# Performance work log

Hardware: AMD Instinct MI355X
Metric: run time of the kernel (lower is better)

The kernel has to match this reference:

```python
import jax, jax.numpy as jnp
import numpy as np

B = 4096        # batch
T = 365         # encoder sequence length
H = 64          # hidden size
HORIZON = 7


def setup_inputs() -> dict:
    key = jax.random.key(0)
    ks = jax.random.split(key, 16)
    s = 0.05
    w = lambda k, shape: (jax.random.normal(k, shape, dtype=jnp.float32) * s)
    return {
        "x": jax.random.normal(ks[0], (B, T, 1), dtype=jnp.float32),
        "enc_Wih0": w(ks[1], (4 * H, 1)),
        "enc_Whh0": w(ks[2], (4 * H, H)),
        "enc_b0": w(ks[3], (4 * H,)),
        "enc_Wih1": w(ks[4], (4 * H, H)),
        "enc_Whh1": w(ks[5], (4 * H, H)),
        "enc_b1": w(ks[6], (4 * H,)),
        "dec_Wih0": w(ks[7], (4 * H, 1)),
        "dec_Whh0": w(ks[8], (4 * H, H)),
        "dec_b0": w(ks[9], (4 * H,)),
        "dec_Wih1": w(ks[10], (4 * H, H)),
        "dec_Whh1": w(ks[11], (4 * H, H)),
        "dec_b1": w(ks[12], (4 * H,)),
        "fc_W": w(ks[13], (1, H)),
        "fc_b": w(ks[14], (1,)),
    }


def _lstm_cell(xt, h, c, Wih, Whh, b):
    # PyTorch gate order: input, forget, cell(g), output
    gates = xt @ Wih.T + h @ Whh.T + b  # [B, 4H]
    i, f, g, o = jnp.split(gates, 4, axis=-1)
    c_new = jax.nn.sigmoid(f) * c + jax.nn.sigmoid(i) * jnp.tanh(g)
    h_new = jax.nn.sigmoid(o) * jnp.tanh(c_new)
    return h_new, c_new


def _run_layer(seq, Wih, Whh, b):
    # seq: [T, B, in] -> hidden seq [T, B, H], final (h, c)
    bsz = seq.shape[1]
    h0 = jnp.zeros((bsz, H), seq.dtype)
    c0 = jnp.zeros((bsz, H), seq.dtype)

    def step(carry, xt):
        h, c = carry
        h, c = _lstm_cell(xt, h, c, Wih, Whh, b)
        return (h, c), h

    (hF, cF), hs = jax.lax.scan(step, (h0, c0), seq)
    return hs, hF, cF


def reference(x, enc_Wih0, enc_Whh0, enc_b0, enc_Wih1, enc_Whh1, enc_b1,
              dec_Wih0, dec_Whh0, dec_b0, dec_Wih1, dec_Whh1, dec_b1,
              fc_W, fc_b):
    xT = jnp.transpose(x, (1, 0, 2))  # [T, B, 1]
    hs0, h0, c0 = _run_layer(xT, enc_Wih0, enc_Whh0, enc_b0)
    _, h1, c1 = _run_layer(hs0, enc_Wih1, enc_Whh1, enc_b1)

    dec_in = jnp.zeros((x.shape[0], 1), x.dtype)  # [B, 1]
    outs = []
    for _ in range(HORIZON):
        h0, c0 = _lstm_cell(dec_in, h0, c0, dec_Wih0, dec_Whh0, dec_b0)
        h1, c1 = _lstm_cell(h0, h1, c1, dec_Wih1, dec_Whh1, dec_b1)
        pred = h1 @ fc_W.T + fc_b  # [B, 1]
        outs.append(pred)
        dec_in = pred
    return jnp.stack(outs, axis=1)  # [B, HORIZON, 1]
```

## Files before the change

kernel.cpp:

```cpp
#include <hip/hip_runtime.h>


typedef _Float16 f16x8 __attribute__((ext_vector_type(8)));
typedef _Float16 f16x4 __attribute__((ext_vector_type(4)));
typedef float    f32x4 __attribute__((ext_vector_type(4)));
typedef float    f32x2 __attribute__((ext_vector_type(2)));

static constexpr int T_ENC = 365;
static constexpr int HZ    = 7;
static constexpr int BT    = 16;
static constexpr int HPAD  = 72;

static constexpr float LOG2E  = 1.442695040888963f;
static constexpr float SCL_I  = -LOG2E;
static constexpr float SCL_G  = 2.0f * LOG2E;

#if __has_builtin(__builtin_amdgcn_exp2f)
__device__ __forceinline__ float fexp2(float x) { return __builtin_amdgcn_exp2f(x); }
#else
__device__ __forceinline__ float fexp2(float x) { return __exp2f(x); }
#endif
#if __has_builtin(__builtin_amdgcn_rcpf)
__device__ __forceinline__ float frcp(float x) { return __builtin_amdgcn_rcpf(x); }
#else
__device__ __forceinline__ float frcp(float x) { return 1.0f / x; }
#endif

__device__ __forceinline__ f32x4 mm1(f16x8 w, f16x8 a, f32x4 acc) {
  return __builtin_amdgcn_mfma_f32_16x16x32_f16(w, a, acc, 0, 0, 0);
}

__global__ __launch_bounds__(512, 2)
void lstm_fused(const float* __restrict__ x,
                const float* __restrict__ eWih0, const float* __restrict__ eWhh0,
                const float* __restrict__ eb0,
                const float* __restrict__ eWih1, const float* __restrict__ eWhh1,
                const float* __restrict__ eb1,
                const float* __restrict__ dWih0, const float* __restrict__ dWhh0,
                const float* __restrict__ db0,
                const float* __restrict__ dWih1, const float* __restrict__ dWhh1,
                const float* __restrict__ db1,
                const float* __restrict__ fcW, const float* __restrict__ fcb,
                float* __restrict__ out)
{
  __shared__ __align__(16) float    xs[T_ENC * BT];
  __shared__ __align__(16) _Float16 h0s[2][BT * HPAD];
  __shared__ __align__(16) _Float16 h1s[2][BT * HPAD];
  __shared__ __align__(16) float    pp[2][16 * 256];
  __shared__ __align__(16) float    dins[BT];

  const int tid  = threadIdx.x;
  const int lane = tid & 63;
  const int wv   = tid >> 6;
  const int wg   = wv & 3;
  const int n    = lane & 15;
  const int q    = lane >> 4;
  const int b0g  = blockIdx.x * BT;
  const int nH   = n * HPAD;
  const int cbase = (wg << 4) + (q << 2);
  const int ppswz = (n & 7) << 2;
  const int ppn   = n << 8;

#if __has_builtin(__builtin_amdgcn_s_setprio)
  if (wv >= 4) __builtin_amdgcn_s_setprio(1);
#endif

  for (int i = tid; i < T_ENC * BT; i += 512) {
    int b = i / T_ENC;
    int t = i - b * T_ENC;
    xs[t * BT + b] = x[(b0g + b) * T_ENC + t];
  }
  for (int i = tid; i < 2 * BT * HPAD; i += 512) {
    ((_Float16*)h0s)[i] = (_Float16)0.f;
    ((_Float16*)h1s)[i] = (_Float16)0.f;
  }
  if (tid < BT) dins[tid] = 0.f;

  f16x8 WA[4][2], WB[4][2], WP[4][2];
  f32x4 biasq[4], wih0q[4], biasqP[4];

  auto gscale = [&](int ti) { return (ti == 2) ? SCL_G : SCL_I; };

  auto cvtrow = [&](const float* p, float s, f16x8& w) {
    #pragma unroll
    for (int j = 0; j < 8; ++j) w[j] = (_Float16)(p[j] * s);
  };
  auto loadA = [&](const float* Wih0_, const float* Whh0_, const float* b0_) {
    #pragma unroll
    for (int ti = 0; ti < 4; ++ti) {
      const float s = gscale(ti);
      const int rw = (ti * 4 + wg) * 16 + n;
      const int rq = (ti * 4 + wg) * 16 + (q << 2);
      #pragma unroll
      for (int rr = 0; rr < 4; ++rr) {
        biasq[ti][rr] = b0_[rq + rr] * s;
        wih0q[ti][rr] = Wih0_[rq + rr] * s;
      }
      #pragma unroll
      for (int kc = 0; kc < 2; ++kc)
        cvtrow(Whh0_ + rw * 64 + kc * 32 + q * 8, s, WA[ti][kc]);
    }
  };
  auto loadAP = [&](const float* Wih1_, const float* b1_) {
    #pragma unroll
    for (int ti = 0; ti < 4; ++ti) {
      const float s = gscale(ti);
      const int rw = (ti * 4 + wg) * 16 + n;
      const int rq = (ti * 4 + wg) * 16 + (q << 2);
      #pragma unroll
      for (int rr = 0; rr < 4; ++rr) biasqP[ti][rr] = b1_[rq + rr] * s;
      #pragma unroll
      for (int kc = 0; kc < 2; ++kc)
        cvtrow(Wih1_ + rw * 64 + kc * 32 + q * 8, s, WP[ti][kc]);
    }
  };
  auto loadB = [&](const float* Wih1_, const float* Whh1_, const float* b1_) {
    #pragma unroll
    for (int ti = 0; ti < 4; ++ti) {
      const float s = gscale(ti);
      const int rw = (ti * 4 + wg) * 16 + n;
      const int rq = (ti * 4 + wg) * 16 + (q << 2);
      #pragma unroll
      for (int rr = 0; rr < 4; ++rr) biasq[ti][rr] = b1_[rq + rr] * s;
      #pragma unroll
      for (int kc = 0; kc < 2; ++kc) {
        cvtrow(Wih1_ + rw * 64 + kc * 32 + q * 8, s, WA[ti][kc]);
        cvtrow(Whh1_ + rw * 64 + kc * 32 + q * 8, s, WB[ti][kc]);
      }
    }
  };

  if (wv < 4) { loadA(eWih0, eWhh0, eb0); loadAP(eWih1, eb1); }
  else        loadB(eWih1, eWhh1, eb1);

  f32x2 cp[2] = {{0.f, 0.f}, {0.f, 0.f}};

  auto act2 = [&](f32x2 a0, f32x2 a1, f32x2 a2, f32x2 a3, f32x2& c) -> f32x2 {
    f32x2 ei, ef, eg, eo;
    ei.x = fexp2(a0.x); ei.y = fexp2(a0.y);
    ef.x = fexp2(a1.x); ef.y = fexp2(a1.y);
    eg.x = fexp2(a2.x); eg.y = fexp2(a2.y);
    eo.x = fexp2(a3.x); eo.y = fexp2(a3.y);
    const f32x2 one = {1.f, 1.f};
    f32x2 di = one + ei, df = one + ef, dg = one + eg, dd = one + eo;
    f32x2 dif = di * df;
    f32x2 dic = di * c;
    f32x2 t1  = dif * dg;
    f32x2 nd  = eg * df - df;
    f32x2 pc  = dic * dg;
    f32x2 s   = pc + nd;
    const f32x2 sclg = {SCL_G, SCL_G};
    f32x2 sg  = sclg * s;
    f32x2 R1; R1.x = frcp(t1.x); R1.y = frcp(t1.y);
    c = R1 * s;
    f32x2 ca = R1 * sg;
    const f32x2 cap = {20.f, 20.f};
    ca.x = fminf(ca.x, cap.x); ca.y = fminf(ca.y, cap.y);
    f32x2 ec; ec.x = fexp2(ca.x); ec.y = fexp2(ca.y);
    f32x2 t2 = ec * dd + dd;
    f32x2 nc = ec - one;
    f32x2 R2; R2.x = frcp(t2.x); R2.y = frcp(t2.y);
    return nc * R2;
  };

  auto epilogue = [&](const f32x4* g, _Float16* O) {
    f32x2 h2[2];
    #pragma unroll
    for (int pr = 0; pr < 2; ++pr) {
      f32x2 a0 = {g[0][2 * pr], g[0][2 * pr + 1]};
      f32x2 a1 = {g[1][2 * pr], g[1][2 * pr + 1]};
      f32x2 a2 = {g[2][2 * pr], g[2][2 * pr + 1]};
      f32x2 a3 = {g[3][2 * pr], g[3][2 * pr + 1]};
      h2[pr] = act2(a0, a1, a2, a3, cp[pr]);
    }
    f16x4 hv;
    hv[0] = (_Float16)h2[0].x; hv[1] = (_Float16)h2[0].y;
    hv[2] = (_Float16)h2[1].x; hv[3] = (_Float16)h2[1].y;
    *(f16x4*)(O + nH + cbase) = hv;
  };

  auto stepA = [&](const _Float16* H, _Float16* O, float xb) {
    const _Float16* hp = H + nH;
    f16x8 a0 = *(const f16x8*)(hp + q * 8);
    f16x8 a1 = *(const f16x8*)(hp + 32 + q * 8);
    const f32x4 xbv = {xb, xb, xb, xb};
    f32x4 g[4];
    #pragma unroll
    for (int ti = 0; ti < 4; ++ti) {
      f32x4 ci = biasq[ti] + xbv * wih0q[ti];
      f32x4 a = mm1(WA[ti][0], a0, ci);
      a = mm1(WA[ti][1], a1, a);
      g[ti] = a;
    }
    epilogue(g, O);
  };

  auto stepAP = [&](const _Float16* H, _Float16* O, float xb, float* ppb) {
    const _Float16* hp = H + nH;
    f16x8 a0 = *(const f16x8*)(hp + q * 8);
    f16x8 a1 = *(const f16x8*)(hp + 32 + q * 8);
    const f32x4 xbv = {xb, xb, xb, xb};
    f32x4 g[4];
    #pragma unroll
    for (int ti = 0; ti < 4; ++ti) {
      f32x4 ci = biasq[ti] + xbv * wih0q[ti];
      f32x4 a = mm1(WA[ti][0], a0, ci);
      a = mm1(WA[ti][1], a1, a);
      g[ti] = a;
    }
    #pragma unroll
    for (int ti = 0; ti < 4; ++ti) {
      f32x4 p = mm1(WP[ti][0], a0, biasqP[ti]);
      p = mm1(WP[ti][1], a1, p);
      const int rq = ((ti * 4 + wg) << 4) + (q << 2);
      *(f32x4*)&ppb[ppn + (rq ^ ppswz)] = p;
    }
    epilogue(g, O);
  };

  auto partialOnly = [&](const _Float16* H, float* ppb) {
    const _Float16* hp = H + nH;
    f16x8 a0 = *(const f16x8*)(hp + q * 8);
    f16x8 a1 = *(const f16x8*)(hp + 32 + q * 8);
    #pragma unroll
    for (int ti = 0; ti < 4; ++ti) {
      f32x4 p = mm1(WP[ti][0], a0, biasqP[ti]);
      p = mm1(WP[ti][1], a1, p);
      const int rq = ((ti * 4 + wg) << 4) + (q << 2);
      *(f32x4*)&ppb[ppn + (rq ^ ppswz)] = p;
    }
  };

  auto stepB_enc = [&](const _Float16* H1, const float* ppb, _Float16* O) {
    const _Float16* p1 = H1 + nH;
    f16x8 a0 = *(const f16x8*)(p1 + q * 8);
    f16x8 a1 = *(const f16x8*)(p1 + 32 + q * 8);
    f32x4 g[4];
    #pragma unroll
    for (int ti = 0; ti < 4; ++ti) {
      const int rq = ((ti * 4 + wg) << 4) + (q << 2);
      f32x4 ci = *(const f32x4*)&ppb[ppn + (rq ^ ppswz)];
      f32x4 a = mm1(WB[ti][0], a0, ci);
      a = mm1(WB[ti][1], a1, a);
      g[ti] = a;
    }
    epilogue(g, O);
  };

  auto stepB = [&](const _Float16* H0, const _Float16* H1, _Float16* O) {
    const _Float16* p0 = H0 + nH;
    const _Float16* p1 = H1 + nH;
    f16x8 b0 = *(const f16x8*)(p0 + q * 8);
    f16x8 b1 = *(const f16x8*)(p0 + 32 + q * 8);
    f16x8 a0 = *(const f16x8*)(p1 + q * 8);
    f16x8 a1 = *(const f16x8*)(p1 + 32 + q * 8);
    f32x4 g[4];
    #pragma unroll
    for (int ti = 0; ti < 4; ++ti) {
      f32x4 a = mm1(WA[ti][0], b0, biasq[ti]);
      a = mm1(WA[ti][1], b1, a);
      a = mm1(WB[ti][0], a0, a);
      a = mm1(WB[ti][1], a1, a);
      g[ti] = a;
    }
    epilogue(g, O);
  };

  __syncthreads();

  float* pp0 = pp[0];
  float* pp1 = pp[1];

  float xb_next;
  if (wv < 4) {
    stepA(h0s[1], h0s[0], xs[n]);
    xb_next = xs[BT + n];
  }
  __syncthreads();
  if (wv < 4) {
    stepAP(h0s[0], h0s[1], xb_next, pp0);
    xb_next = xs[2 * BT + n];
  }
  __syncthreads();

  for (int s = 2; s <= 362; s += 2) {
    if (wv < 4) {
      stepAP(h0s[1], h0s[0], xb_next, pp1);
      xb_next = xs[(s + 1) * BT + n];
    } else {
      stepB_enc(h1s[1], pp0, h1s[0]);
    }
    __syncthreads();
    if (wv < 4) {
      stepAP(h0s[0], h0s[1], xb_next, pp0);
      xb_next = xs[(s + 2) * BT + n];
    } else {
      stepB_enc(h1s[0], pp1, h1s[1]);
    }
    __syncthreads();
  }

  if (wv < 4) stepAP(h0s[1], h0s[0], xb_next, pp1);
  else        stepB_enc(h1s[1], pp0, h1s[0]);
  __syncthreads();
  if (wv < 4) partialOnly(h0s[0], pp0);
  else        stepB_enc(h1s[0], pp1, h1s[1]);
  __syncthreads();
  if (wv < 4) loadA(dWih0, dWhh0, db0);
  else        stepB_enc(h1s[1], pp0, h1s[0]);
  __syncthreads();

  if (wv >= 4) loadB(dWih1, dWhh1, db1);
  float fcw[16];
  #pragma unroll
  for (int j = 0; j < 16; ++j) fcw[j] = fcW[q * 16 + j];
  const float fcb0 = fcb[0];

  #pragma unroll 1
  for (int hz = 0; hz < HZ; ++hz) {
    const int p = hz & 1;
    if (wv < 4) {
      stepA(h0s[p], h0s[1 - p], dins[n]);
    }
    __syncthreads();
    if (wv >= 4) {
      stepB(h0s[1 - p], h1s[p], h1s[1 - p]);
    }
    __syncthreads();
    if (wv == 0) {
      const _Float16* Hh = h1s[1 - p];
      f16x8 hh0 = *(const f16x8*)(Hh + nH + q * 16);
      f16x8 hh1 = *(const f16x8*)(Hh + nH + q * 16 + 8);
      float pacc = 0.f;
      #pragma unroll
      for (int j = 0; j < 8; ++j) pacc += fcw[j] * (float)hh0[j];
      #pragma unroll
      for (int j = 0; j < 8; ++j) pacc += fcw[8 + j] * (float)hh1[j];
      pacc += __shfl_down(pacc, 32);
      pacc += __shfl_down(pacc, 16);
      if (lane < BT) {
        pacc += fcb0;
        out[(b0g + lane) * HZ + hz] = pacc;
        dins[lane] = pacc;
      }
    }
    __syncthreads();
  }
}

extern "C" void kernel_launch(void* const* d_in, const int* in_sizes, int n_in,
                              void* d_out, int out_size, void* d_ws, size_t ws_size,
                              hipStream_t stream) {
  (void)in_sizes; (void)n_in; (void)d_ws; (void)ws_size; (void)out_size;
  const float* x     = (const float*)d_in[0];
  const float* eWih0 = (const float*)d_in[1];
  const float* eWhh0 = (const float*)d_in[2];
  const float* eb0   = (const float*)d_in[3];
  const float* eWih1 = (const float*)d_in[4];
  const float* eWhh1 = (const float*)d_in[5];
  const float* eb1   = (const float*)d_in[6];
  const float* dWih0 = (const float*)d_in[7];
  const float* dWhh0 = (const float*)d_in[8];
  const float* db0   = (const float*)d_in[9];
  const float* dWih1 = (const float*)d_in[10];
  const float* dWhh1 = (const float*)d_in[11];
  const float* db1   = (const float*)d_in[12];
  const float* fcW   = (const float*)d_in[13];
  const float* fcb   = (const float*)d_in[14];
  float* out = (float*)d_out;

  dim3 grid(4096 / BT);
  dim3 block(512);
  hipLaunchKernelGGL(lstm_fused, grid, block, 0, stream,
                     x, eWih0, eWhh0, eb0, eWih1, eWhh1, eb1,
                     dWih0, dWhh0, db0, dWih1, dWhh1, db1, fcW, fcb, out);
}
```

Measured before the change: 323.5 us.

## Split layer-1 input projection into a third wave group of 768-thread blocks

Block size grows from 512 to 768 threads. A new group of four waves computes the layer-1 input projection (Wih1·h0 plus bias) into the shared partial buffer, so the layer-0 waves only run their own recurrence step and register use per wave drops (WP/biasqP removed, weights share a WX slot). This shortens the per-step critical path of the layer-0 waves. The costs are more waves contending for the MFMA units and barriers, launch bounds of 768×3 that may limit registers or occupancy, and a setprio change that now raises priority for waves 0–7.

```diff
diff --git a/kernel.cpp b/kernel.cpp
--- a/kernel.cpp
+++ b/kernel.cpp
@@ -30,7 +30,7 @@
   return __builtin_amdgcn_mfma_f32_16x16x32_f16(w, a, acc, 0, 0, 0);
 }
 
-__global__ __launch_bounds__(512, 2)
+__global__ __launch_bounds__(768, 3)
 void lstm_fused(const float* __restrict__ x,
                 const float* __restrict__ eWih0, const float* __restrict__ eWhh0,
                 const float* __restrict__ eb0,
@@ -62,22 +62,22 @@
   const int ppn   = n << 8;
 
 #if __has_builtin(__builtin_amdgcn_s_setprio)
-  if (wv >= 4) __builtin_amdgcn_s_setprio(1);
+  if (wv < 8) __builtin_amdgcn_s_setprio(1);
 #endif
 
-  for (int i = tid; i < T_ENC * BT; i += 512) {
+  for (int i = tid; i < T_ENC * BT; i += 768) {
     int b = i / T_ENC;
     int t = i - b * T_ENC;
     xs[t * BT + b] = x[(b0g + b) * T_ENC + t];
   }
-  for (int i = tid; i < 2 * BT * HPAD; i += 512) {
+  for (int i = tid; i < 2 * BT * HPAD; i += 768) {
     ((_Float16*)h0s)[i] = (_Float16)0.f;
     ((_Float16*)h1s)[i] = (_Float16)0.f;
   }
   if (tid < BT) dins[tid] = 0.f;
 
-  f16x8 WA[4][2], WB[4][2], WP[4][2];
-  f32x4 biasq[4], wih0q[4], biasqP[4];
+  f16x8 WA[4][2], WX[4][2];
+  f32x4 biasq[4], wih0q[4];
 
   auto gscale = [&](int ti) { return (ti == 2) ? SCL_G : SCL_I; };
 
@@ -101,17 +101,27 @@
         cvtrow(Whh0_ + rw * 64 + kc * 32 + q * 8, s, WA[ti][kc]);
     }
   };
-  auto loadAP = [&](const float* Wih1_, const float* b1_) {
+  auto loadWhh = [&](const float* Whh1_) {
+    #pragma unroll
+    for (int ti = 0; ti < 4; ++ti) {
+      const float s = gscale(ti);
+      const int rw = (ti * 4 + wg) * 16 + n;
+      #pragma unroll
+      for (int kc = 0; kc < 2; ++kc)
+        cvtrow(Whh1_ + rw * 64 + kc * 32 + q * 8, s, WX[ti][kc]);
+    }
+  };
+  auto loadWP = [&](const float* Wih1_, const float* b1_) {
     #pragma unroll
     for (int ti = 0; ti < 4; ++ti) {
       const float s = gscale(ti);
       const int rw = (ti * 4 + wg) * 16 + n;
       const int rq = (ti * 4 + wg) * 16 + (q << 2);
       #pragma unroll
-      for (int rr = 0; rr < 4; ++rr) biasqP[ti][rr] = b1_[rq + rr] * s;
+      for (int rr = 0; rr < 4; ++rr) biasq[ti][rr] = b1_[rq + rr] * s;
       #pragma unroll
       for (int kc = 0; kc < 2; ++kc)
-        cvtrow(Wih1_ + rw * 64 + kc * 32 + q * 8, s, WP[ti][kc]);
+        cvtrow(Wih1_ + rw * 64 + kc * 32 + q * 8, s, WX[ti][kc]);
     }
   };
   auto loadB = [&](const float* Wih1_, const float* Whh1_, const float* b1_) {
@@ -125,13 +135,14 @@
       #pragma unroll
       for (int kc = 0; kc < 2; ++kc) {
         cvtrow(Wih1_ + rw * 64 + kc * 32 + q * 8, s, WA[ti][kc]);
-        cvtrow(Whh1_ + rw * 64 + kc * 32 + q * 8, s, WB[ti][kc]);
+        cvtrow(Whh1_ + rw * 64 + kc * 32 + q * 8, s, WX[ti][kc]);
       }
     }
   };
 
-  if (wv < 4) { loadA(eWih0, eWhh0, eb0); loadAP(eWih1, eb1); }
-  else        loadB(eWih1, eWhh1, eb1);
+  if (wv < 4)      loadA(eWih0, eWhh0, eb0);
+  else if (wv < 8) loadWhh(eWhh1);
+  else             loadWP(eWih1, eb1);
 
   f32x2 cp[2] = {{0.f, 0.f}, {0.f, 0.f}};
 
@@ -195,43 +206,20 @@
     epilogue(g, O);
   };
 
-  auto stepAP = [&](const _Float16* H, _Float16* O, float xb, float* ppb) {
+  auto stepP = [&](const _Float16* H, float* ppb) {
     const _Float16* hp = H + nH;
     f16x8 a0 = *(const f16x8*)(hp + q * 8);
     f16x8 a1 = *(const f16x8*)(hp + 32 + q * 8);
-    const f32x4 xbv = {xb, xb, xb, xb};
-    f32x4 g[4];
-    #pragma unroll
-    for (int ti = 0; ti < 4; ++ti) {
-      f32x4 ci = biasq[ti] + xbv * wih0q[ti];
-      f32x4 a = mm1(WA[ti][0], a0, ci);
-      a = mm1(WA[ti][1], a1, a);
-      g[ti] = a;
-    }
-    #pragma unroll
-    for (int ti = 0; ti < 4; ++ti) {
-      f32x4 p = mm1(WP[ti][0], a0, biasqP[ti]);
-      p = mm1(WP[ti][1], a1, p);
+    #pragma unroll
+    for (int ti = 0; ti < 4; ++ti) {
+      f32x4 p = mm1(WX[ti][0], a0, biasq[ti]);
+      p = mm1(WX[ti][1], a1, p);
       const int rq = ((ti * 4 + wg) << 4) + (q << 2);
       *(f32x4*)&ppb[ppn + (rq ^ ppswz)] = p;
     }
-    epilogue(g, O);
-  };
-
-  auto partialOnly = [&](const _Float16* H, float* ppb) {
-    const _Float16* hp = H + nH;
-    f16x8 a0 = *(const f16x8*)(hp + q * 8);
-    f16x8 a1 = *(const f16x8*)(hp + 32 + q * 8);
-    #pragma unroll
-    for (int ti = 0; ti < 4; ++ti) {
-      f32x4 p = mm1(WP[ti][0], a0, biasqP[ti]);
-      p = mm1(WP[ti][1], a1, p);
-      const int rq = ((ti * 4 + wg) << 4) + (q << 2);
-      *(f32x4*)&ppb[ppn + (rq ^ ppswz)] = p;
-    }
-  };
-
-  auto stepB_enc = [&](const _Float16* H1, const float* ppb, _Float16* O) {
+  };
+
+  auto stepB2 = [&](const _Float16* H1, const float* ppb, _Float16* O) {
     const _Float16* p1 = H1 + nH;
     f16x8 a0 = *(const f16x8*)(p1 + q * 8);
     f16x8 a1 = *(const f16x8*)(p1 + 32 + q * 8);
@@ -240,8 +228,8 @@
     for (int ti = 0; ti < 4; ++ti) {
       const int rq = ((ti * 4 + wg) << 4) + (q << 2);
       f32x4 ci = *(const f32x4*)&ppb[ppn + (rq ^ ppswz)];
-      f32x4 a = mm1(WB[ti][0], a0, ci);
-      a = mm1(WB[ti][1], a1, a);
+      f32x4 a = mm1(WX[ti][0], a0, ci);
+      a = mm1(WX[ti][1], a1, a);
       g[ti] = a;
     }
     epilogue(g, O);
@@ -259,8 +247,8 @@
     for (int ti = 0; ti < 4; ++ti) {
       f32x4 a = mm1(WA[ti][0], b0, biasq[ti]);
       a = mm1(WA[ti][1], b1, a);
-      a = mm1(WB[ti][0], a0, a);
-      a = mm1(WB[ti][1], a1, a);
+      a = mm1(WX[ti][0], a0, a);
+      a = mm1(WX[ti][1], a1, a);
       g[ti] = a;
     }
     epilogue(g, O);
@@ -278,39 +266,46 @@
   }
   __syncthreads();
   if (wv < 4) {
-    stepAP(h0s[0], h0s[1], xb_next, pp0);
+    stepA(h0s[0], h0s[1], xb_next);
     xb_next = xs[2 * BT + n];
-  }
-  __syncthreads();
-
-  for (int s = 2; s <= 362; s += 2) {
+  } else if (wv >= 8) {
+    stepP(h0s[0], pp0);
+  }
+  __syncthreads();
+
+  for (int u = 2; u <= 362; u += 2) {
     if (wv < 4) {
-      stepAP(h0s[1], h0s[0], xb_next, pp1);
-      xb_next = xs[(s + 1) * BT + n];
+      stepA(h0s[1], h0s[0], xb_next);
+      xb_next = xs[(u + 1) * BT + n];
+    } else if (wv < 8) {
+      stepB2(h1s[1], pp0, h1s[0]);
     } else {
-      stepB_enc(h1s[1], pp0, h1s[0]);
+      stepP(h0s[1], pp1);
     }
     __syncthreads();
     if (wv < 4) {
-      stepAP(h0s[0], h0s[1], xb_next, pp0);
-      xb_next = xs[(s + 2) * BT + n];
+      stepA(h0s[0], h0s[1], xb_next);
+      xb_next = xs[(u + 2) * BT + n];
+    } else if (wv < 8) {
+      stepB2(h1s[0], pp1, h1s[1]);
     } else {
-      stepB_enc(h1s[0], pp1, h1s[1]);
-    }
-    __syncthreads();
-  }
-
-  if (wv < 4) stepAP(h0s[1], h0s[0], xb_next, pp1);
-  else        stepB_enc(h1s[1], pp0, h1s[0]);
-  __syncthreads();
-  if (wv < 4) partialOnly(h0s[0], pp0);
-  else        stepB_enc(h1s[0], pp1, h1s[1]);
-  __syncthreads();
-  if (wv < 4) loadA(dWih0, dWhh0, db0);
-  else        stepB_enc(h1s[1], pp0, h1s[0]);
-  __syncthreads();
-
-  if (wv >= 4) loadB(dWih1, dWhh1, db1);
+      stepP(h0s[0], pp0);
+    }
+    __syncthreads();
+  }
+
+  if (wv < 4)      stepA(h0s[1], h0s[0], xb_next);
+  else if (wv < 8) stepB2(h1s[1], pp0, h1s[0]);
+  else             stepP(h0s[1], pp1);
+  __syncthreads();
+  if (wv < 4)      loadA(dWih0, dWhh0, db0);
+  else if (wv < 8) stepB2(h1s[0], pp1, h1s[1]);
+  else             stepP(h0s[0], pp0);
+  __syncthreads();
+  if (wv >= 4 && wv < 8) stepB2(h1s[1], pp0, h1s[0]);
+  __syncthreads();
+
+  if (wv >= 4 && wv < 8) loadB(dWih1, dWhh1, db1);
   float fcw[16];
   #pragma unroll
   for (int j = 0; j < 16; ++j) fcw[j] = fcW[q * 16 + j];
@@ -323,7 +318,7 @@
       stepA(h0s[p], h0s[1 - p], dins[n]);
     }
     __syncthreads();
-    if (wv >= 4) {
+    if (wv >= 4 && wv < 8) {
       stepB(h0s[1 - p], h1s[p], h1s[1 - p]);
     }
     __syncthreads();
@@ -370,7 +365,7 @@
   float* out = (float*)d_out;
 
   dim3 grid(4096 / BT);
-  dim3 block(512);
+  dim3 block(768);
   hipLaunchKernelGGL(lstm_fused, grid, block, 0, stream,
                      x, eWih0, eWhh0, eb0, eWih1, eWhh1, eb1,
                      dWih0, dWhh0, db0, dWih1, dWhh1, db1, fcW, fcb, out);
```

New measurement: 312.6 us. -3.4%, faster.
